# Optimization experiments

Measured on AMD Instinct MI355X. Metric: run time of the kernel, lower is better.

Reference implementation:

```python
import jax, jax.numpy as jnp
import numpy as np

HIDDEN = 1024
EMB = HIDDEN // 2          # embedding_dim = hidden_dim // 2
NUM_OPS = 8
BATCH = 16384


def setup_inputs() -> dict:
    key = jax.random.key(0)
    ks = jax.random.split(key, 8)
    x = jax.random.normal(ks[0], (BATCH, HIDDEN), dtype=jnp.float32)
    sampled_ops = jax.random.randint(ks[1], (BATCH,), 0, NUM_OPS, dtype=jnp.int32)
    op_emb = jax.random.normal(ks[2], (NUM_OPS, EMB), dtype=jnp.float32) * 0.02
    # per-expert 2-layer MLP params (Linear stored as [in, out] for x @ W)
    s1 = 1.0 / np.sqrt(HIDDEN + EMB)
    s2 = 1.0 / np.sqrt(HIDDEN)
    W1 = jax.random.uniform(ks[3], (NUM_OPS, HIDDEN + EMB, HIDDEN), jnp.float32, -s1, s1)
    b1 = jax.random.uniform(ks[4], (NUM_OPS, HIDDEN), jnp.float32, -s1, s1)
    W2 = jax.random.uniform(ks[5], (NUM_OPS, HIDDEN, HIDDEN), jnp.float32, -s2, s2)
    b2 = jax.random.uniform(ks[6], (NUM_OPS, HIDDEN), jnp.float32, -s2, s2)
    return {"x": x, "sampled_ops": sampled_ops, "op_emb": op_emb,
            "W1": W1, "b1": b1, "W2": W2, "b2": b2}


def reference(x, sampled_ops, op_emb, W1, b1, W2, b2):
    # gather per-token operator embedding and augment input
    emb = jnp.take(op_emb, sampled_ops, axis=0)            # [B, EMB]
    x_aug = jnp.concatenate([x, emb], axis=-1)             # [B, H+EMB]
    num_ops = W1.shape[0]
    out = jnp.zeros_like(x)
    # loop over the small fixed expert set; mask-combine per token
    for o in range(num_ops):
        h = jax.nn.relu(x_aug @ W1[o] + b1[o])             # [B, H]
        y = jax.nn.relu(h @ W2[o] + b2[o])                 # [B, H]
        mask = (sampled_ops == o)[:, None]
        out = out + jnp.where(mask, y, 0.0)
    return out
```

## Files before the change

kernel.cpp:

```cpp
#include <hip/hip_runtime.h>
#include <hip/hip_bf16.h>

#define BATCH 16384
#define HID   1024
#define EMBD  512
#define NOPS  8
#define MAXT  136
#define CNTS  16

typedef __attribute__((ext_vector_type(8))) short bf16x8;
typedef __attribute__((ext_vector_type(4))) float f32x4;

__device__ __forceinline__ unsigned short f2bf(float f) {
  unsigned int u = __float_as_uint(f);
  u += 0x7FFF + ((u >> 16) & 1);
  return (unsigned short)(u >> 16);
}

__device__ __forceinline__ unsigned int pk2(float a, float b) {
  __hip_bfloat162 t = __float22bfloat162_rn(make_float2(a, b));
  return *(unsigned int*)(&t);
}

__device__ __forceinline__ void lds_load16(void* lds, const void* g) {
  __builtin_amdgcn_global_load_lds(
      (const __attribute__((address_space(1))) unsigned int*)g,
      (__attribute__((address_space(3))) unsigned int*)lds, 16, 0, 0);
}

__device__ __forceinline__ void decode_bid(int bid, int& g, int& nx) {
  g = 17 * (bid & 7) + (bid >> 6);
  nx = (bid >> 3) & 7;
}

__global__ void bucket_k(const int* __restrict__ ops, int* __restrict__ cnt,
                         int* __restrict__ idx) {
  __shared__ int wcnt[4][NOPS];
  __shared__ int wbase[4][NOPS];
  int tid = threadIdx.x, lane = tid & 63, w = tid >> 6;
  int t = blockIdx.x * 256 + tid;
  int op = ops[t];
  unsigned long long msave = 0;
#pragma unroll
  for (int o = 0; o < NOPS; ++o) {
    unsigned long long mm = __ballot(op == o);
    if (op == o) msave = mm;
    if (lane == o) wcnt[w][o] = __popcll(mm);
  }
  __syncthreads();
  if (tid < NOPS) {
    int c0 = wcnt[0][tid], c1 = wcnt[1][tid], c2 = wcnt[2][tid], c3 = wcnt[3][tid];
    int base = atomicAdd(&cnt[tid * CNTS], c0 + c1 + c2 + c3);
    wbase[0][tid] = base;
    wbase[1][tid] = base + c0;
    wbase[2][tid] = base + c0 + c1;
    wbase[3][tid] = base + c0 + c1 + c2;
  }
  __syncthreads();
  int pre = __popcll(msave & ((1ull << lane) - 1ull));
  idx[op * BATCH + wbase[w][op] + pre] = t;
}

__global__ void schedule_k(const int* __restrict__ cnt, int* __restrict__ desc,
                           int* __restrict__ ntp, int* __restrict__ idx) {
  if (threadIdx.x == 0) {
    int n = 0;
    for (int e = 0; e < NOPS; ++e) {
      int c = cnt[e * CNTS];
      for (int t = 0; t < c; t += 128) { desc[2 * n] = e; desc[2 * n + 1] = t; ++n; }
    }
    *ntp = n;
  }
  for (int e = 0; e < NOPS; ++e) {
    int c = cnt[e * CNTS];
    int cp = (c + 127) & ~127;
    for (int p = c + (int)threadIdx.x; p < cp; p += 256) idx[e * BATCH + p] = 0;
  }
}

__global__ void prep_k(const float* __restrict__ W1, const float* __restrict__ W2,
                       short* __restrict__ W1p, short* __restrict__ W2p,
                       const float* __restrict__ x, const float* __restrict__ emb,
                       const int* __restrict__ idx, const int* __restrict__ desc,
                       const int* __restrict__ ntp, short* __restrict__ Ap) {
  int bid = blockIdx.x;
  int tid = threadIdx.x;

  if (bid >= 5120) {
    __shared__ int toks[128];
    int bid2 = bid - 5120;
    int g = bid2 / 12, kx = bid2 % 12;
    if (g >= *ntp) return;
    int e = desc[2 * g], rs = desc[2 * g + 1];
    if (tid < 128) toks[tid] = idx[e * BATCH + rs + tid];
    __syncthreads();
    int r = tid >> 1, ah = tid & 1;
    int tok = toks[r];
    short* dst0 = Ap + (size_t)g * 48 * 4096;
#pragma unroll
    for (int kk = 0; kk < 4; ++kk) {
      int ks = kx * 4 + kk;
      const float* src = (ks < 32) ? (x + (size_t)tok * HID + ks * 32 + ah * 16)
                                   : (emb + e * EMBD + (ks - 32) * 32 + ah * 16);
      float4 f0 = ((const float4*)src)[0];
      float4 f1 = ((const float4*)src)[1];
      float4 f2v = ((const float4*)src)[2];
      float4 f3 = ((const float4*)src)[3];
      uint4 p0 = make_uint4(pk2(f0.x, f0.y), pk2(f0.z, f0.w), pk2(f1.x, f1.y), pk2(f1.z, f1.w));
      uint4 p1 = make_uint4(pk2(f2v.x, f2v.y), pk2(f2v.z, f2v.w), pk2(f3.x, f3.y), pk2(f3.z, f3.w));
      short* dst = dst0 + ks * 4096 + r * 32 + ah * 16;
      ((uint4*)dst)[0] = p0;
      ((uint4*)dst)[1] = p1;
    }
    return;
  }

  const float* W; short* Wp; int ks, nx;
  if (bid < 3072) {
    int e = bid / 384; int r = bid % 384; nx = r / 48; ks = r % 48;
    W = W1 + (size_t)e * 1536 * 1024;
    Wp = W1p + ((size_t)(e * 8 + nx) * 48 + ks) * 4096;
  } else {
    int b = bid - 3072;
    int e = b / 256; int r = b % 256; nx = r / 32; ks = r % 32;
    W = W2 + (size_t)e * 1024 * 1024;
    Wp = W2p + ((size_t)(e * 8 + nx) * 32 + ks) * 4096;
  }
  int n = tid & 127, kh = tid >> 7;
  const float* src = W + (size_t)(ks * 32 + kh * 16) * 1024 + nx * 128 + n;
  float v[16];
#pragma unroll
  for (int kk = 0; kk < 16; ++kk) v[kk] = src[(size_t)kk * 1024];
  uint4 a, b;
  a.x = pk2(v[0], v[1]);  a.y = pk2(v[2], v[3]);
  a.z = pk2(v[4], v[5]);  a.w = pk2(v[6], v[7]);
  b.x = pk2(v[8], v[9]);  b.y = pk2(v[10], v[11]);
  b.z = pk2(v[12], v[13]); b.w = pk2(v[14], v[15]);
  uint4* dst = (uint4*)(Wp + (size_t)n * 32);
  dst[kh * 2] = a;
  dst[kh * 2 + 1] = b;
}

__global__ __launch_bounds__(256) void gemm1_k(
    const short* __restrict__ Ap, const float* __restrict__ b1,
    const short* __restrict__ W1p, unsigned short* __restrict__ hp,
    const int* __restrict__ desc, const int* __restrict__ ntp) {
  int g, nx;
  decode_bid(blockIdx.x, g, nx);
  if (g >= *ntp) return;
  int e = desc[2 * g];

  __shared__ __align__(16) char smem[16384];
  short* lA = (short*)smem;
  short* lB = (short*)(smem + 8192);

  int tid = threadIdx.x, lane = tid & 63, w = tid >> 6;
  int wm = w >> 1, wn = w & 1;
  int fr = lane & 15, fq = lane >> 4;

  const char* Asrc = (const char*)Ap + (size_t)g * 48 * 8192;
  const char* Bsrc = (const char*)W1p + (size_t)(e * 8 + nx) * 48 * 8192;

  f32x4 acc[4][4] = {};

  for (int ks = 0; ks < 48; ++ks) {
    const char* as = Asrc + ks * 8192;
    const char* bs = Bsrc + ks * 8192;
    lds_load16(smem + w * 1024, as + w * 1024 + lane * 16);
    lds_load16(smem + 4096 + w * 1024, as + 4096 + w * 1024 + lane * 16);
    lds_load16(smem + 8192 + w * 1024, bs + w * 1024 + lane * 16);
    lds_load16(smem + 12288 + w * 1024, bs + 4096 + w * 1024 + lane * 16);
    __syncthreads();

    bf16x8 af[4], bfr[4];
#pragma unroll
    for (int i = 0; i < 4; ++i)
      af[i] = *(const bf16x8*)&lA[(wm * 64 + i * 16 + fr) * 32 + fq * 8];
#pragma unroll
    for (int j = 0; j < 4; ++j)
      bfr[j] = *(const bf16x8*)&lB[(wn * 64 + j * 16 + fr) * 32 + fq * 8];
#pragma unroll
    for (int i = 0; i < 4; ++i)
#pragma unroll
      for (int j = 0; j < 4; ++j)
        acc[i][j] = __builtin_amdgcn_mfma_f32_16x16x32_bf16(af[i], bfr[j], acc[i][j], 0, 0, 0);
    __syncthreads();
  }

  float bias[4];
#pragma unroll
  for (int j = 0; j < 4; ++j)
    bias[j] = b1[e * HID + nx * 128 + wn * 64 + j * 16 + fr];

  unsigned short* ls = (unsigned short*)smem;
  int lr = lane >> 2;
#pragma unroll
  for (int i = 0; i < 4; ++i) {
    __syncthreads();
#pragma unroll
    for (int j = 0; j < 4; ++j)
#pragma unroll
      for (int rg = 0; rg < 4; ++rg) {
        float v = acc[i][j][rg] + bias[j];
        v = v > 0.f ? v : 0.f;
        ls[w * 1024 + (fq * 4 + rg) * 64 + j * 16 + fr] = f2bf(v);
      }
    __syncthreads();
    int R = wm * 64 + i * 16 + lr;
#pragma unroll
    for (int s = 0; s < 2; ++s) {
      int ch = (lane & 3) + s * 4;
      int ks2 = nx * 4 + wn * 2 + (ch >> 2);
      uint4 val = *(const uint4*)&ls[w * 1024 + lr * 64 + ch * 8];
      *(uint4*)(hp + ((size_t)(g * 32 + ks2) * 128 + R) * 32 + (ch & 3) * 8) = val;
    }
  }
}

__global__ __launch_bounds__(256) void gemm2_k(
    const unsigned short* __restrict__ hp, const float* __restrict__ b2,
    const short* __restrict__ W2p, float* __restrict__ out,
    const int* __restrict__ idx, const int* __restrict__ cnt,
    const int* __restrict__ desc, const int* __restrict__ ntp) {
  int g, nx;
  decode_bid(blockIdx.x, g, nx);
  if (g >= *ntp) return;
  int e = desc[2 * g], rs = desc[2 * g + 1];
  int ce = cnt[e * CNTS];

  __shared__ __align__(16) char smem[16384];
  __shared__ int toks[128];
  short* lA = (short*)smem;
  short* lB = (short*)(smem + 8192);

  int tid = threadIdx.x, lane = tid & 63, w = tid >> 6;
  int wm = w >> 1, wn = w & 1;
  int fr = lane & 15, fq = lane >> 4;

  if (tid < 128) toks[tid] = idx[e * BATCH + rs + tid];

  const char* Asrc = (const char*)hp + (size_t)g * 32 * 8192;
  const char* Bsrc = (const char*)W2p + (size_t)(e * 8 + nx) * 32 * 8192;

  f32x4 acc[4][4] = {};

  for (int ks = 0; ks < 32; ++ks) {
    const char* as = Asrc + ks * 8192;
    const char* bs = Bsrc + ks * 8192;
    lds_load16(smem + w * 1024, as + w * 1024 + lane * 16);
    lds_load16(smem + 4096 + w * 1024, as + 4096 + w * 1024 + lane * 16);
    lds_load16(smem + 8192 + w * 1024, bs + w * 1024 + lane * 16);
    lds_load16(smem + 12288 + w * 1024, bs + 4096 + w * 1024 + lane * 16);
    __syncthreads();

    bf16x8 af[4], bfr[4];
#pragma unroll
    for (int i = 0; i < 4; ++i)
      af[i] = *(const bf16x8*)&lA[(wm * 64 + i * 16 + fr) * 32 + fq * 8];
#pragma unroll
    for (int j = 0; j < 4; ++j)
      bfr[j] = *(const bf16x8*)&lB[(wn * 64 + j * 16 + fr) * 32 + fq * 8];
#pragma unroll
    for (int i = 0; i < 4; ++i)
#pragma unroll
      for (int j = 0; j < 4; ++j)
        acc[i][j] = __builtin_amdgcn_mfma_f32_16x16x32_bf16(af[i], bfr[j], acc[i][j], 0, 0, 0);
    __syncthreads();
  }

  float bias[4];
#pragma unroll
  for (int j = 0; j < 4; ++j)
    bias[j] = b2[e * HID + nx * 128 + wn * 64 + j * 16 + fr];

  float* lsf = (float*)smem;
  int lr = lane >> 2;
#pragma unroll
  for (int i = 0; i < 4; ++i) {
    __syncthreads();
#pragma unroll
    for (int j = 0; j < 4; ++j)
#pragma unroll
      for (int rg = 0; rg < 4; ++rg) {
        float v = acc[i][j][rg] + bias[j];
        lsf[w * 1024 + (fq * 4 + rg) * 64 + j * 16 + fr] = v > 0.f ? v : 0.f;
      }
    __syncthreads();
    int R = wm * 64 + i * 16 + lr;
    if (R < ce - rs) {
      float* orow = out + (size_t)toks[R] * HID + nx * 128 + wn * 64;
#pragma unroll
      for (int s = 0; s < 4; ++s) {
        int ch = (lane & 3) + s * 4;
        *(float4*)(orow + ch * 4) = *(const float4*)&lsf[w * 1024 + lr * 64 + ch * 4];
      }
    }
  }
}


extern "C" void kernel_launch(void* const* d_in, const int* in_sizes, int n_in,
                              void* d_out, int out_size, void* d_ws, size_t ws_size,
                              hipStream_t stream) {
  const float* x   = (const float*)d_in[0];
  const int*   ops = (const int*)d_in[1];
  const float* emb = (const float*)d_in[2];
  const float* W1  = (const float*)d_in[3];
  const float* b1  = (const float*)d_in[4];
  const float* W2  = (const float*)d_in[5];
  const float* b2  = (const float*)d_in[6];
  float* out = (float*)d_out;

  char* ws = (char*)d_ws;
  int* cnt  = (int*)(ws + 0);
  int* ntp  = (int*)(ws + 1024);
  int* desc = (int*)(ws + 1280);
  int* idx  = (int*)(ws + 4096);
  short* W1p = (short*)(ws + 528384);
  short* W2p = (short*)(ws + 25694208);
  unsigned short* hp = (unsigned short*)(ws + 42471424);
  short* Ap = (short*)(ws + 78123008);

  hipMemsetAsync(cnt, 0, 512, stream);
  bucket_k<<<BATCH / 256, 256, 0, stream>>>(ops, cnt, idx);
  schedule_k<<<1, 256, 0, stream>>>(cnt, desc, ntp, idx);
  prep_k<<<5120 + 12 * MAXT, 256, 0, stream>>>(W1, W2, W1p, W2p,
                                               x, emb, idx, desc, ntp, Ap);
  gemm1_k<<<8 * MAXT, 256, 0, stream>>>(Ap, b1, W1p, hp, desc, ntp);
  gemm2_k<<<8 * MAXT, 256, 0, stream>>>(hp, b2, W2p, out, idx, cnt, desc, ntp);
}
```

Baseline: 338.9 us.

## Overlap weight conversion with bucketing and gemm1 via merged kernel grids

Splits the monolithic prep kernel so that W1 bf16 conversion runs in the same grid as token bucketing, and W2 conversion runs as extra blocks appended to the gemm1 grid. The aim is to fill idle CUs during the small bucket launch and during gemm1's tail with independent weight-packing work. The risk is that the extra blocks in the gemm1 grid contend for memory bandwidth and CU slots with the GEMM blocks. Block scheduling order decides whether the W2 work actually overlaps or just runs after the GEMM.

```diff
diff --git a/kernel.cpp b/kernel.cpp
--- a/kernel.cpp
+++ b/kernel.cpp
@@ -33,12 +33,40 @@
   nx = (bid >> 3) & 7;
 }
 
-__global__ void bucket_k(const int* __restrict__ ops, int* __restrict__ cnt,
-                         int* __restrict__ idx) {
+__device__ __forceinline__ void w_prep_tile(const float* __restrict__ W,
+                                            short* __restrict__ Wp,
+                                            int ks, int nx, int tid) {
+  int n = tid & 127, kh = tid >> 7;
+  const float* src = W + (size_t)(ks * 32 + kh * 16) * 1024 + nx * 128 + n;
+  float v[16];
+#pragma unroll
+  for (int kk = 0; kk < 16; ++kk) v[kk] = src[(size_t)kk * 1024];
+  uint4 a, b;
+  a.x = pk2(v[0], v[1]);  a.y = pk2(v[2], v[3]);
+  a.z = pk2(v[4], v[5]);  a.w = pk2(v[6], v[7]);
+  b.x = pk2(v[8], v[9]);  b.y = pk2(v[10], v[11]);
+  b.z = pk2(v[12], v[13]); b.w = pk2(v[14], v[15]);
+  uint4* dst = (uint4*)(Wp + (size_t)n * 32);
+  dst[kh * 2] = a;
+  dst[kh * 2 + 1] = b;
+}
+
+__global__ void bucket_w1_k(const int* __restrict__ ops, int* __restrict__ cnt,
+                            int* __restrict__ idx, const float* __restrict__ W1,
+                            short* __restrict__ W1p) {
+  int bid = blockIdx.x;
+  int tid = threadIdx.x;
+  if (bid >= 64) {
+    int b = bid - 64;
+    int e = b / 384; int r = b % 384; int nx = r / 48, ks = r % 48;
+    w_prep_tile(W1 + (size_t)e * 1536 * 1024,
+                W1p + ((size_t)(e * 8 + nx) * 48 + ks) * 4096, ks, nx, tid);
+    return;
+  }
   __shared__ int wcnt[4][NOPS];
   __shared__ int wbase[4][NOPS];
-  int tid = threadIdx.x, lane = tid & 63, w = tid >> 6;
-  int t = blockIdx.x * 256 + tid;
+  int lane = tid & 63, w = tid >> 6;
+  int t = bid * 256 + tid;
   int op = ops[t];
   unsigned long long msave = 0;
 #pragma unroll
@@ -78,75 +106,53 @@
   }
 }
 
-__global__ void prep_k(const float* __restrict__ W1, const float* __restrict__ W2,
-                       short* __restrict__ W1p, short* __restrict__ W2p,
-                       const float* __restrict__ x, const float* __restrict__ emb,
-                       const int* __restrict__ idx, const int* __restrict__ desc,
-                       const int* __restrict__ ntp, short* __restrict__ Ap) {
+__global__ void prep_a_k(const float* __restrict__ x, const float* __restrict__ emb,
+                         const int* __restrict__ idx, const int* __restrict__ desc,
+                         const int* __restrict__ ntp, short* __restrict__ Ap) {
+  __shared__ int toks[128];
+  int bid = blockIdx.x;
+  int g = bid / 12, kx = bid % 12;
+  if (g >= *ntp) return;
+  int e = desc[2 * g], rs = desc[2 * g + 1];
+  int tid = threadIdx.x;
+  if (tid < 128) toks[tid] = idx[e * BATCH + rs + tid];
+  __syncthreads();
+  int r = tid >> 1, ah = tid & 1;
+  int tok = toks[r];
+  short* dst0 = Ap + (size_t)g * 48 * 4096;
+#pragma unroll
+  for (int kk = 0; kk < 4; ++kk) {
+    int ks = kx * 4 + kk;
+    const float* src = (ks < 32) ? (x + (size_t)tok * HID + ks * 32 + ah * 16)
+                                 : (emb + e * EMBD + (ks - 32) * 32 + ah * 16);
+    float4 f0 = ((const float4*)src)[0];
+    float4 f1 = ((const float4*)src)[1];
+    float4 f2v = ((const float4*)src)[2];
+    float4 f3 = ((const float4*)src)[3];
+    uint4 p0 = make_uint4(pk2(f0.x, f0.y), pk2(f0.z, f0.w), pk2(f1.x, f1.y), pk2(f1.z, f1.w));
+    uint4 p1 = make_uint4(pk2(f2v.x, f2v.y), pk2(f2v.z, f2v.w), pk2(f3.x, f3.y), pk2(f3.z, f3.w));
+    short* dst = dst0 + ks * 4096 + r * 32 + ah * 16;
+    ((uint4*)dst)[0] = p0;
+    ((uint4*)dst)[1] = p1;
+  }
+}
+
+__global__ __launch_bounds__(256) void gemm1_w2_k(
+    const short* __restrict__ Ap, const float* __restrict__ b1,
+    const short* __restrict__ W1p, unsigned short* __restrict__ hp,
+    const int* __restrict__ desc, const int* __restrict__ ntp,
+    const float* __restrict__ W2, short* __restrict__ W2p) {
   int bid = blockIdx.x;
   int tid = threadIdx.x;
-
-  if (bid >= 5120) {
-    __shared__ int toks[128];
-    int bid2 = bid - 5120;
-    int g = bid2 / 12, kx = bid2 % 12;
-    if (g >= *ntp) return;
-    int e = desc[2 * g], rs = desc[2 * g + 1];
-    if (tid < 128) toks[tid] = idx[e * BATCH + rs + tid];
-    __syncthreads();
-    int r = tid >> 1, ah = tid & 1;
-    int tok = toks[r];
-    short* dst0 = Ap + (size_t)g * 48 * 4096;
-#pragma unroll
-    for (int kk = 0; kk < 4; ++kk) {
-      int ks = kx * 4 + kk;
-      const float* src = (ks < 32) ? (x + (size_t)tok * HID + ks * 32 + ah * 16)
-                                   : (emb + e * EMBD + (ks - 32) * 32 + ah * 16);
-      float4 f0 = ((const float4*)src)[0];
-      float4 f1 = ((const float4*)src)[1];
-      float4 f2v = ((const float4*)src)[2];
-      float4 f3 = ((const float4*)src)[3];
-      uint4 p0 = make_uint4(pk2(f0.x, f0.y), pk2(f0.z, f0.w), pk2(f1.x, f1.y), pk2(f1.z, f1.w));
-      uint4 p1 = make_uint4(pk2(f2v.x, f2v.y), pk2(f2v.z, f2v.w), pk2(f3.x, f3.y), pk2(f3.z, f3.w));
-      short* dst = dst0 + ks * 4096 + r * 32 + ah * 16;
-      ((uint4*)dst)[0] = p0;
-      ((uint4*)dst)[1] = p1;
-    }
+  if (bid >= 8 * MAXT) {
+    int b = bid - 8 * MAXT;
+    int e = b / 256; int r = b % 256; int nx = r / 32, ks = r % 32;
+    w_prep_tile(W2 + (size_t)e * 1024 * 1024,
+                W2p + ((size_t)(e * 8 + nx) * 32 + ks) * 4096, ks, nx, tid);
     return;
   }
-
-  const float* W; short* Wp; int ks, nx;
-  if (bid < 3072) {
-    int e = bid / 384; int r = bid % 384; nx = r / 48; ks = r % 48;
-    W = W1 + (size_t)e * 1536 * 1024;
-    Wp = W1p + ((size_t)(e * 8 + nx) * 48 + ks) * 4096;
-  } else {
-    int b = bid - 3072;
-    int e = b / 256; int r = b % 256; nx = r / 32; ks = r % 32;
-    W = W2 + (size_t)e * 1024 * 1024;
-    Wp = W2p + ((size_t)(e * 8 + nx) * 32 + ks) * 4096;
-  }
-  int n = tid & 127, kh = tid >> 7;
-  const float* src = W + (size_t)(ks * 32 + kh * 16) * 1024 + nx * 128 + n;
-  float v[16];
-#pragma unroll
-  for (int kk = 0; kk < 16; ++kk) v[kk] = src[(size_t)kk * 1024];
-  uint4 a, b;
-  a.x = pk2(v[0], v[1]);  a.y = pk2(v[2], v[3]);
-  a.z = pk2(v[4], v[5]);  a.w = pk2(v[6], v[7]);
-  b.x = pk2(v[8], v[9]);  b.y = pk2(v[10], v[11]);
-  b.z = pk2(v[12], v[13]); b.w = pk2(v[14], v[15]);
-  uint4* dst = (uint4*)(Wp + (size_t)n * 32);
-  dst[kh * 2] = a;
-  dst[kh * 2 + 1] = b;
-}
-
-__global__ __launch_bounds__(256) void gemm1_k(
-    const short* __restrict__ Ap, const float* __restrict__ b1,
-    const short* __restrict__ W1p, unsigned short* __restrict__ hp,
-    const int* __restrict__ desc, const int* __restrict__ ntp) {
   int g, nx;
-  decode_bid(blockIdx.x, g, nx);
+  decode_bid(bid, g, nx);
   if (g >= *ntp) return;
   int e = desc[2 * g];
 
@@ -154,7 +160,7 @@
   short* lA = (short*)smem;
   short* lB = (short*)(smem + 8192);
 
-  int tid = threadIdx.x, lane = tid & 63, w = tid >> 6;
+  int lane = tid & 63, w = tid >> 6;
   int wm = w >> 1, wn = w & 1;
   int fr = lane & 15, fq = lane >> 4;
 
@@ -322,10 +328,9 @@
   short* Ap = (short*)(ws + 78123008);
 
   hipMemsetAsync(cnt, 0, 512, stream);
-  bucket_k<<<BATCH / 256, 256, 0, stream>>>(ops, cnt, idx);
+  bucket_w1_k<<<64 + 3072, 256, 0, stream>>>(ops, cnt, idx, W1, W1p);
   schedule_k<<<1, 256, 0, stream>>>(cnt, desc, ntp, idx);
-  prep_k<<<5120 + 12 * MAXT, 256, 0, stream>>>(W1, W2, W1p, W2p,
-                                               x, emb, idx, desc, ntp, Ap);
-  gemm1_k<<<8 * MAXT, 256, 0, stream>>>(Ap, b1, W1p, hp, desc, ntp);
+  prep_a_k<<<12 * MAXT, 256, 0, stream>>>(x, emb, idx, desc, ntp, Ap);
+  gemm1_w2_k<<<8 * MAXT + 2048, 256, 0, stream>>>(Ap, b1, W1p, hp, desc, ntp, W2, W2p);
   gemm2_k<<<8 * MAXT, 256, 0, stream>>>(hp, b2, W2p, out, idx, cnt, desc, ntp);
 }
```

Result: faster. 325.0 us (-4.1%).
